# Performance work log

Hardware: AMD Instinct MI355X
Metric: run time of the kernel (lower is better)

The kernel has to match this reference:

```python
import jax, jax.numpy as jnp
import numpy as np

# R-FCN PSRoI pooling constants (match init_kwargs)
P = 7          # pooled_height == pooled_width
GS = 7         # group_size
D = 21         # output_dim
SCALE = 0.0625 # spatial_scale (1/16)


def setup_inputs() -> dict:
    key = jax.random.key(0)
    k1, k2, k3, k4 = jax.random.split(key, 4)
    N, C, H, W = 4, D * GS * GS, 80, 80   # C = output_dim * group_size^2
    R = 2048
    features = jax.random.normal(k1, (N, C, H, W), dtype=jnp.float32)
    img = H / SCALE  # 1280 px image
    bidx = jax.random.randint(k2, (R,), 0, N).astype(jnp.float32)
    xy1 = jax.random.uniform(k3, (R, 2), minval=0.0, maxval=img * 0.6)
    wh = jax.random.uniform(k4, (R, 2), minval=img * 0.05, maxval=img * 0.4)
    xy2 = jnp.clip(xy1 + wh, 0.0, img - 1.0)
    rois = jnp.concatenate([bidx[:, None], xy1, xy2], axis=1)  # [R,5]: (b,x1,y1,x2,y2)
    return {"features": features, "rois": rois}


def reference(features, rois):
    """Position-sensitive RoI pooling (R-FCN psroi_pooling_forward_cuda semantics).

    Each output bin (ctop, ph, pw) averages feature channel
    c = (ctop*GS + gh)*GS + gw over the bin's integer pixel region.
    Bin sums are computed exactly via a 2D integral image, turning the
    irregular per-bin reduction into 4 gathers per bin.
    """
    N, C, H, W = features.shape
    R = rois.shape[0]

    # Integral image: ii[n,c,i,j] = sum of features[n,c,:i,:j]; shape [N,C,H+1,W+1]
    ii = jnp.pad(
        jnp.cumsum(jnp.cumsum(features, axis=2), axis=3),
        ((0, 0), (0, 0), (1, 0), (1, 0)),
    )

    b = rois[:, 0].astype(jnp.int32)                       # [R]
    x1 = jnp.round(rois[:, 1]) * SCALE
    y1 = jnp.round(rois[:, 2]) * SCALE
    x2 = (jnp.round(rois[:, 3]) + 1.0) * SCALE
    y2 = (jnp.round(rois[:, 4]) + 1.0) * SCALE
    bin_w = jnp.maximum(x2 - x1, 0.1) / P                  # [R]
    bin_h = jnp.maximum(y2 - y1, 0.1) / P

    g = jnp.arange(P, dtype=jnp.float32)                   # bin index grid
    hs = jnp.clip(jnp.floor(g[None, :] * bin_h[:, None] + y1[:, None]), 0, H).astype(jnp.int32)        # [R,P]
    he = jnp.clip(jnp.ceil((g[None, :] + 1.0) * bin_h[:, None] + y1[:, None]), 0, H).astype(jnp.int32)
    ws = jnp.clip(jnp.floor(g[None, :] * bin_w[:, None] + x1[:, None]), 0, W).astype(jnp.int32)
    we = jnp.clip(jnp.ceil((g[None, :] + 1.0) * bin_w[:, None] + x1[:, None]), 0, W).astype(jnp.int32)

    # Position-sensitive channel map: c[ctop,ph,pw] = (ctop*GS+gh)*GS+gw
    ctop = jnp.arange(D)[:, None, None]
    gh = jnp.clip((jnp.arange(P) * GS) // P, 0, GS - 1)[None, :, None]
    gw = jnp.clip((jnp.arange(P) * GS) // P, 0, GS - 1)[None, None, :]
    cmap = (ctop * GS + gh) * GS + gw                      # [D,P,P]

    # Broadcast gather indices to [R,D,P,P]
    B = b[:, None, None, None]
    Cc = cmap[None]
    HS = hs[:, None, :, None]; HE = he[:, None, :, None]
    WS = ws[:, None, None, :]; WE = we[:, None, None, :]

    s = ii[B, Cc, HE, WE] - ii[B, Cc, HS, WE] - ii[B, Cc, HE, WS] + ii[B, Cc, HS, WS]
    area = ((HE - HS) * (WE - WS)).astype(features.dtype)
    out = jnp.where(area > 0, s / jnp.maximum(area, 1.0), jnp.zeros((), features.dtype))
    return out  # [R, D, P, P]
```

## Files before the change

### kernel.cpp

```cpp
#include <hip/hip_runtime.h>

#define P   7
#define GS  7
#define D   21
#define HH  80
#define WW  80
#define CC  (D * GS * GS)
#define PLANE (HH * WW)
#define IW  84
#define NSEG 5
#define SEGLEN 16

__device__ __forceinline__ float recip7() {
    union { unsigned u; float f; } c; c.u = 0x3E124925u; return c.f;
}

__device__ __forceinline__ float mul_add_nofma(float a, float b, float c) {
    float t = a * b;
    asm volatile("" : "+v"(t));
    return t + c;
}

__global__ __launch_bounds__(1024) void prep_kernel(
    const float* __restrict__ rois, int R, int N,
    unsigned short* __restrict__ hshe,
    unsigned short* __restrict__ wswe,
    int* __restrict__ jlist, int* __restrict__ base)
{
    __shared__ unsigned char bsh[2048];
    __shared__ int wcnt[16][8];
    __shared__ int wbase[16][8];
    __shared__ int baseS[9];
    int tid = threadIdx.x, wave = tid >> 6, lane = tid & 63;

    for (int r = tid; r < R; r += 1024) {
        const float* roi = rois + (size_t)r * 5;
        bsh[r] = (unsigned char)(int)roi[0];

        float x1 = rintf(roi[1]) * 0.0625f;
        float y1 = rintf(roi[2]) * 0.0625f;
        float x2 = (rintf(roi[3]) + 1.0f) * 0.0625f;
        float y2 = (rintf(roi[4]) + 1.0f) * 0.0625f;
        float bin_w = fmaxf(x2 - x1, 0.1f) * recip7();
        float bin_h = fmaxf(y2 - y1, 0.1f) * recip7();
        asm volatile("" : "+v"(bin_w), "+v"(bin_h));

        #pragma unroll
        for (int g = 0; g < 7; ++g) {
            float hs_f = floorf(mul_add_nofma((float)g,       bin_h, y1));
            float he_f = ceilf (mul_add_nofma((float)(g + 1), bin_h, y1));
            float ws_f = floorf(mul_add_nofma((float)g,       bin_w, x1));
            float we_f = ceilf (mul_add_nofma((float)(g + 1), bin_w, x1));
            int hs = (int)fminf(fmaxf(hs_f, 0.0f), 80.0f);
            int he = (int)fminf(fmaxf(he_f, 0.0f), 80.0f);
            int ws = (int)fminf(fmaxf(ws_f, 0.0f), 80.0f);
            int we = (int)fminf(fmaxf(we_f, 0.0f), 80.0f);
            hshe[r * 7 + g] = (unsigned short)(hs | (he << 8));
            wswe[r * 7 + g] = (unsigned short)(ws | (we << 8));
        }
    }
    __syncthreads();

    int chunk = (R + 15) / 16;
    int rbeg = wave * chunk;
    int rend = min(rbeg + chunk, R);
    int cnt[8];
    #pragma unroll
    for (int b = 0; b < 8; ++b) cnt[b] = 0;
    for (int rr = rbeg + lane; rr < rend; rr += 64) {
        int bv = bsh[rr];
        #pragma unroll
        for (int b = 0; b < 8; ++b) {
            if (b < N) cnt[b] += __popcll(__ballot(bv == b));
        }
    }
    if (lane == 0) {
        #pragma unroll
        for (int b = 0; b < 8; ++b) wcnt[wave][b] = cnt[b];
    }
    __syncthreads();

    if (tid < 8) {
        int b = tid, acc = 0;
        for (int w = 0; w < 16; ++w) { wbase[w][b] = acc; acc += wcnt[w][b]; }
        baseS[b] = acc;
    }
    __syncthreads();
    if (tid == 0) {
        int acc = 0;
        for (int b = 0; b < N; ++b) { int t = baseS[b]; baseS[b] = acc; acc += t; }
        baseS[N] = acc;
    }
    __syncthreads();

    {
        int off[8];
        #pragma unroll
        for (int b = 0; b < 8; ++b) off[b] = (b < N) ? (baseS[b] + wbase[wave][b]) : 0;
        for (int rr = rbeg + lane; rr < rend; rr += 64) {
            int bv = bsh[rr];
            #pragma unroll
            for (int b = 0; b < 8; ++b) {
                if (b < N) {
                    unsigned long long mask = __ballot(bv == b);
                    if (bv == b) {
                        int pos = off[b] + __popcll(mask & ((1ull << lane) - 1ull));
                        jlist[pos] = rr;
                    }
                    off[b] += __popcll(mask);
                }
            }
        }
    }
    if (tid <= N) base[tid] = baseS[tid];
}

__global__ __launch_bounds__(512) void psroi_plane_kernel(
    const float* __restrict__ feat, int R,
    const unsigned short* __restrict__ hshe,
    const unsigned short* __restrict__ wswe,
    const int* __restrict__ jlist, const int* __restrict__ base,
    float* __restrict__ dst)
{
    __shared__ float ii[HH * IW];
    __shared__ float tot[NSEG][HH];

    int tid = threadIdx.x;
    int bid = blockIdx.x;
    int b   = bid / CC;
    int c   = bid % CC;
    int rem = c % (GS * GS);
    int gh  = rem / GS;
    int gw  = rem % GS;

    const float4* src4 = (const float4*)(feat + ((size_t)b * CC + c) * PLANE);
    for (int i = tid; i < PLANE / 4; i += 512) {
        float4 v = src4[i];
        int h = i / 20;
        int w = (i % 20) * 4;
        *(float4*)(&ii[h * IW + w]) = v;
    }

    int j0 = base[b], j1 = base[b + 1];
    int jA = j0 + tid, jB = jA + 512, jC = jA + 1024, jD = jA + 1536;
    int rA = (jA < j1) ? jlist[jA] : 0;
    int rB = (jB < j1) ? jlist[jB] : 0;
    int rC = (jC < j1) ? jlist[jC] : 0;
    int rD = (jD < j1) ? jlist[jD] : 0;
    unsigned hA = (jA < j1) ? hshe[rA * 7 + gh] : 0;
    unsigned wA = (jA < j1) ? wswe[rA * 7 + gw] : 0;
    unsigned hB = (jB < j1) ? hshe[rB * 7 + gh] : 0;
    unsigned wB = (jB < j1) ? wswe[rB * 7 + gw] : 0;
    unsigned hC = (jC < j1) ? hshe[rC * 7 + gh] : 0;
    unsigned wC = (jC < j1) ? wswe[rC * 7 + gw] : 0;
    unsigned hD = (jD < j1) ? hshe[rD * 7 + gh] : 0;
    unsigned wD = (jD < j1) ? wswe[rD * 7 + gw] : 0;

    __syncthreads();

    bool act = tid < NSEG * WW;
    int seg = tid / WW;
    int lw  = tid % WW;

    {
        float v[SEGLEN];
        int col = lw, h0 = seg * SEGLEN;
        if (act) {
            float s = 0.0f;
            #pragma unroll
            for (int k = 0; k < SEGLEN; ++k) { v[k] = ii[(h0 + k) * IW + col]; s += v[k]; }
            tot[seg][lw] = s;
        }
        __syncthreads();
        if (act) {
            float off = 0.0f;
            #pragma unroll
            for (int jj = 0; jj < NSEG - 1; ++jj) if (jj < seg) off += tot[jj][lw];
            float run = off;
            #pragma unroll
            for (int k = 0; k < SEGLEN; ++k) { run += v[k]; ii[(h0 + k) * IW + col] = run; }
        }
        __syncthreads();
    }
    {
        float4 q0, q1, q2, q3;
        int row = lw, w0 = seg * SEGLEN;
        float4* rp = (float4*)&ii[row * IW + w0];
        if (act) {
            q0 = rp[0]; q1 = rp[1]; q2 = rp[2]; q3 = rp[3];
            float s = (((((q0.x + q0.y) + (q0.z + q0.w))
                       + ((q1.x + q1.y) + (q1.z + q1.w)))
                      + (((q2.x + q2.y) + (q2.z + q2.w))
                       + ((q3.x + q3.y) + (q3.z + q3.w)))));
            s = q0.x; s += q0.y; s += q0.z; s += q0.w;
            s += q1.x; s += q1.y; s += q1.z; s += q1.w;
            s += q2.x; s += q2.y; s += q2.z; s += q2.w;
            s += q3.x; s += q3.y; s += q3.z; s += q3.w;
            tot[seg][row] = s;
        }
        __syncthreads();
        if (act) {
            float off = 0.0f;
            #pragma unroll
            for (int jj = 0; jj < NSEG - 1; ++jj) if (jj < seg) off += tot[jj][row];
            float run = off;
            run += q0.x; q0.x = run; run += q0.y; q0.y = run;
            run += q0.z; q0.z = run; run += q0.w; q0.w = run;
            run += q1.x; q1.x = run; run += q1.y; q1.y = run;
            run += q1.z; q1.z = run; run += q1.w; q1.w = run;
            run += q2.x; q2.x = run; run += q2.y; q2.y = run;
            run += q2.z; q2.z = run; run += q2.w; q2.w = run;
            run += q3.x; q3.x = run; run += q3.y; q3.y = run;
            run += q3.z; q3.z = run; run += q3.w; q3.w = run;
            rp[0] = q0; rp[1] = q1; rp[2] = q2; rp[3] = q3;
        }
        __syncthreads();
    }

    #define IIV(hq, wq) ( ((hq) > 0 && (wq) > 0)                              \
        ? ii[((hq) - 1) * IW + ((wq) - 1)] : 0.0f )
    #define EMIT(jX, hX, wX)                                                  \
    if (jX < j1) {                                                            \
        int hs = hX & 255, he = (int)(hX >> 8);                               \
        int ws = wX & 255, we = (int)(wX >> 8);                               \
        float s = ((IIV(he, we) - IIV(hs, we))                                \
                 -  IIV(he, ws)) + IIV(hs, ws);                               \
        int area = (he - hs) * (we - ws);                                     \
        dst[(size_t)c * R + jX] = (area > 0) ? (s / (float)area) : 0.0f;      \
    }
    EMIT(jA, hA, wA)
    EMIT(jB, hB, wB)
    EMIT(jC, hC, wC)
    EMIT(jD, hD, wD)
    #undef EMIT
    #undef IIV
}

__global__ __launch_bounds__(256) void transpose_kernel(
    const float* __restrict__ in, const int* __restrict__ jlist,
    float* __restrict__ out, int R, int C)
{
    __shared__ float t[64][65];
    __shared__ int rows[64];
    int j0 = blockIdx.x * 64;
    int c0 = blockIdx.y * 64;
    int tx = threadIdx.x, ty = threadIdx.y;
    int tid = ty * 64 + tx;

    if (tid < 64 && j0 + tid < R) rows[tid] = jlist[j0 + tid];

    #pragma unroll
    for (int k0 = 0; k0 < 64; k0 += 4) {
        int k = k0 + ty;
        int cc = c0 + k, jj = j0 + tx;
        if (cc < C && jj < R) t[k][tx] = in[(size_t)cc * R + jj];
    }
    __syncthreads();
    #pragma unroll
    for (int k0 = 0; k0 < 64; k0 += 4) {
        int k = k0 + ty;
        int cc = c0 + tx;
        if (j0 + k < R && cc < C) out[(size_t)rows[k] * C + cc] = t[tx][k];
    }
}

__global__ __launch_bounds__(256) void psroi_fallback_kernel(
    const float* __restrict__ feat, const float* __restrict__ rois,
    int R, float* __restrict__ out)
{
    __shared__ float ii[81 * 81];
    int bid = blockIdx.x;
    int b = bid / CC, c = bid % CC;
    int rem = c % 49, gh = rem / 7, gw = rem % 7;

    const float* plane = feat + ((size_t)b * CC + c) * PLANE;
    for (int i = threadIdx.x; i < PLANE; i += 256) {
        int h = i / WW, w = i % WW;
        ii[(h + 1) * 81 + (w + 1)] = plane[i];
    }
    for (int i = threadIdx.x; i < 81; i += 256) { ii[i] = 0.0f; ii[i * 81] = 0.0f; }
    __syncthreads();
    if (threadIdx.x < WW) {
        int w = threadIdx.x + 1; float s = 0.0f;
        for (int h = 1; h <= HH; ++h) { s += ii[h * 81 + w]; ii[h * 81 + w] = s; }
    }
    __syncthreads();
    if (threadIdx.x < HH) {
        int h = threadIdx.x + 1; float* row = &ii[h * 81]; float s = 0.0f;
        for (int w = 1; w <= WW; ++w) { s += row[w]; row[w] = s; }
    }
    __syncthreads();
    for (int r = threadIdx.x; r < R; r += 256) {
        const float* roi = rois + (size_t)r * 5;
        if ((int)roi[0] != b) continue;
        float x1 = rintf(roi[1]) * 0.0625f;
        float y1 = rintf(roi[2]) * 0.0625f;
        float x2 = (rintf(roi[3]) + 1.0f) * 0.0625f;
        float y2 = (rintf(roi[4]) + 1.0f) * 0.0625f;
        float bw = fmaxf(x2 - x1, 0.1f) * recip7();
        float bh = fmaxf(y2 - y1, 0.1f) * recip7();
        asm volatile("" : "+v"(bw), "+v"(bh));
        int hs = (int)fminf(fmaxf(floorf(mul_add_nofma((float)gh,     bh, y1)), 0.0f), 80.0f);
        int he = (int)fminf(fmaxf(ceilf (mul_add_nofma((float)(gh+1), bh, y1)), 0.0f), 80.0f);
        int ws = (int)fminf(fmaxf(floorf(mul_add_nofma((float)gw,     bw, x1)), 0.0f), 80.0f);
        int we = (int)fminf(fmaxf(ceilf (mul_add_nofma((float)(gw+1), bw, x1)), 0.0f), 80.0f);
        float s = ii[he * 81 + we] - ii[hs * 81 + we] - ii[he * 81 + ws] + ii[hs * 81 + ws];
        int area = (he - hs) * (we - ws);
        out[(size_t)r * CC + c] = (area > 0) ? (s / (float)area) : 0.0f;
    }
}

extern "C" void kernel_launch(void* const* d_in, const int* in_sizes, int n_in,
                              void* d_out, int out_size, void* d_ws, size_t ws_size,
                              hipStream_t stream)
{
    const float* feat = (const float*)d_in[0];
    const float* rois = (const float*)d_in[1];
    float* out        = (float*)d_out;

    int R = in_sizes[1] / 5;
    int N = in_sizes[0] / (CC * PLANE);

    size_t off_wsT  = 0;
    size_t off_hshe = (off_wsT + (size_t)CC * R * sizeof(float) + 15) & ~(size_t)15;
    size_t off_wswe = off_hshe + (size_t)R * 7 * sizeof(unsigned short);
    size_t off_jl   = (off_wswe + (size_t)R * 7 * sizeof(unsigned short) + 15) & ~(size_t)15;
    size_t off_base = off_jl + (size_t)R * sizeof(int);
    size_t need     = off_base + (size_t)(N + 1) * sizeof(int);

    bool chunk_ok = (((R + 15) / 16) % 64) == 0;

    if (ws_size >= need && N <= 8 && R <= 2048 && chunk_ok) {
        char* ws = (char*)d_ws;
        float*          ws_T = (float*)(ws + off_wsT);
        unsigned short* hshe = (unsigned short*)(ws + off_hshe);
        unsigned short* wswe = (unsigned short*)(ws + off_wswe);
        int*            jl   = (int*)(ws + off_jl);
        int*            base = (int*)(ws + off_base);

        prep_kernel<<<1, 1024, 0, stream>>>(rois, R, N, hshe, wswe, jl, base);
        psroi_plane_kernel<<<N * CC, 512, 0, stream>>>(feat, R, hshe, wswe, jl, base, ws_T);
        dim3 blk(64, 4), grd((R + 63) / 64, (CC + 63) / 64);
        transpose_kernel<<<grd, blk, 0, stream>>>(ws_T, jl, out, R, CC);
    } else {
        psroi_fallback_kernel<<<N * CC, 256, 0, stream>>>(feat, rois, R, out);
    }
}
```

Baseline: 45.58 us.

## Make plane kernel persistent with double-buffered async global-to-LDS loads

Replaces the one-block-per-plane launch with 512 persistent blocks that each loop over several feature planes. The next plane is prefetched into a second LDS buffer with global_load_lds while the current plane is scanned and its bins are gathered. Barriers are replaced by manual s_waitcnt plus s_barrier. The aim is to hide global load latency behind the scan and gather work. In exchange LDS use per block roughly doubles, which lowers occupancy, and correctness now depends on hand-placed vmcnt waits.

```diff
diff --git a/kernel.cpp b/kernel.cpp
--- a/kernel.cpp
+++ b/kernel.cpp
@@ -10,6 +10,10 @@
 #define IW  84
 #define NSEG 5
 #define SEGLEN 16
+#define NBLK 512
+#define BUFQ 2048
+#define BUFF (BUFQ * 4)
+#define REALQ 1680
 
 __device__ __forceinline__ float recip7() {
     union { unsigned u; float f; } c; c.u = 0x3E124925u; return c.f;
@@ -19,6 +23,28 @@
     float t = a * b;
     asm volatile("" : "+v"(t));
     return t + c;
+}
+
+#define MEMFENCE() asm volatile("" ::: "memory")
+#define LGKM_BAR() do { asm volatile("s_waitcnt lgkmcnt(0)" ::: "memory"); \
+                        __builtin_amdgcn_s_barrier(); MEMFENCE(); } while (0)
+
+__device__ __forceinline__ void gll16(const float* g, float* l) {
+    __builtin_amdgcn_global_load_lds(
+        (const __attribute__((address_space(1))) void*)g,
+        (__attribute__((address_space(3))) void*)l, 16, 0, 0);
+}
+
+__device__ __forceinline__ void stage_issue(const float* plane, float* buf, int tid) {
+    #pragma unroll
+    for (int k = 0; k < 4; ++k) {
+        int q0 = (tid & ~63) + k * 512;
+        int q  = q0 + (tid & 63);
+        int row = q / 21, w4 = q - row * 21;
+        const float* src = (q < REALQ && w4 < 20) ? (plane + row * WW + w4 * 4)
+                                                  : plane;
+        gll16(src, buf + q0 * 4);
+    }
 }
 
 __global__ __launch_bounds__(1024) void prep_kernel(
@@ -116,124 +142,129 @@
 }
 
 __global__ __launch_bounds__(512) void psroi_plane_kernel(
-    const float* __restrict__ feat, int R,
+    const float* __restrict__ feat, int R, int NPLANES,
     const unsigned short* __restrict__ hshe,
     const unsigned short* __restrict__ wswe,
     const int* __restrict__ jlist, const int* __restrict__ base,
     float* __restrict__ dst)
 {
-    __shared__ float ii[HH * IW];
+    __shared__ float bufA[BUFF];
+    __shared__ float bufB[BUFF];
     __shared__ float tot[NSEG][HH];
 
     int tid = threadIdx.x;
     int bid = blockIdx.x;
-    int b   = bid / CC;
-    int c   = bid % CC;
-    int rem = c % (GS * GS);
-    int gh  = rem / GS;
-    int gw  = rem % GS;
-
-    const float4* src4 = (const float4*)(feat + ((size_t)b * CC + c) * PLANE);
-    for (int i = tid; i < PLANE / 4; i += 512) {
-        float4 v = src4[i];
-        int h = i / 20;
-        int w = (i % 20) * 4;
-        *(float4*)(&ii[h * IW + w]) = v;
-    }
-
-    int j0 = base[b], j1 = base[b + 1];
-    int jA = j0 + tid, jB = jA + 512, jC = jA + 1024, jD = jA + 1536;
-    int rA = (jA < j1) ? jlist[jA] : 0;
-    int rB = (jB < j1) ? jlist[jB] : 0;
-    int rC = (jC < j1) ? jlist[jC] : 0;
-    int rD = (jD < j1) ? jlist[jD] : 0;
-    unsigned hA = (jA < j1) ? hshe[rA * 7 + gh] : 0;
-    unsigned wA = (jA < j1) ? wswe[rA * 7 + gw] : 0;
-    unsigned hB = (jB < j1) ? hshe[rB * 7 + gh] : 0;
-    unsigned wB = (jB < j1) ? wswe[rB * 7 + gw] : 0;
-    unsigned hC = (jC < j1) ? hshe[rC * 7 + gh] : 0;
-    unsigned wC = (jC < j1) ? wswe[rC * 7 + gw] : 0;
-    unsigned hD = (jD < j1) ? hshe[rD * 7 + gh] : 0;
-    unsigned wD = (jD < j1) ? wswe[rD * 7 + gw] : 0;
-
-    __syncthreads();
+
+    stage_issue(feat + (size_t)bid * PLANE, bufA, tid);
 
     bool act = tid < NSEG * WW;
     int seg = tid / WW;
     int lw  = tid % WW;
 
-    {
-        float v[SEGLEN];
-        int col = lw, h0 = seg * SEGLEN;
-        if (act) {
-            float s = 0.0f;
-            #pragma unroll
-            for (int k = 0; k < SEGLEN; ++k) { v[k] = ii[(h0 + k) * IW + col]; s += v[k]; }
-            tot[seg][lw] = s;
-        }
-        __syncthreads();
-        if (act) {
-            float off = 0.0f;
-            #pragma unroll
-            for (int jj = 0; jj < NSEG - 1; ++jj) if (jj < seg) off += tot[jj][lw];
-            float run = off;
-            #pragma unroll
-            for (int k = 0; k < SEGLEN; ++k) { run += v[k]; ii[(h0 + k) * IW + col] = run; }
-        }
-        __syncthreads();
-    }
-    {
-        float4 q0, q1, q2, q3;
-        int row = lw, w0 = seg * SEGLEN;
-        float4* rp = (float4*)&ii[row * IW + w0];
-        if (act) {
-            q0 = rp[0]; q1 = rp[1]; q2 = rp[2]; q3 = rp[3];
-            float s = (((((q0.x + q0.y) + (q0.z + q0.w))
-                       + ((q1.x + q1.y) + (q1.z + q1.w)))
-                      + (((q2.x + q2.y) + (q2.z + q2.w))
-                       + ((q3.x + q3.y) + (q3.z + q3.w)))));
-            s = q0.x; s += q0.y; s += q0.z; s += q0.w;
-            s += q1.x; s += q1.y; s += q1.z; s += q1.w;
-            s += q2.x; s += q2.y; s += q2.z; s += q2.w;
-            s += q3.x; s += q3.y; s += q3.z; s += q3.w;
-            tot[seg][row] = s;
-        }
-        __syncthreads();
-        if (act) {
-            float off = 0.0f;
-            #pragma unroll
-            for (int jj = 0; jj < NSEG - 1; ++jj) if (jj < seg) off += tot[jj][row];
-            float run = off;
-            run += q0.x; q0.x = run; run += q0.y; q0.y = run;
-            run += q0.z; q0.z = run; run += q0.w; q0.w = run;
-            run += q1.x; q1.x = run; run += q1.y; q1.y = run;
-            run += q1.z; q1.z = run; run += q1.w; q1.w = run;
-            run += q2.x; q2.x = run; run += q2.y; q2.y = run;
-            run += q2.z; q2.z = run; run += q2.w; q2.w = run;
-            run += q3.x; q3.x = run; run += q3.y; q3.y = run;
-            run += q3.z; q3.z = run; run += q3.w; q3.w = run;
-            rp[0] = q0; rp[1] = q1; rp[2] = q2; rp[3] = q3;
-        }
-        __syncthreads();
-    }
-
-    #define IIV(hq, wq) ( ((hq) > 0 && (wq) > 0)                              \
-        ? ii[((hq) - 1) * IW + ((wq) - 1)] : 0.0f )
-    #define EMIT(jX, hX, wX)                                                  \
-    if (jX < j1) {                                                            \
-        int hs = hX & 255, he = (int)(hX >> 8);                               \
-        int ws = wX & 255, we = (int)(wX >> 8);                               \
-        float s = ((IIV(he, we) - IIV(hs, we))                                \
-                 -  IIV(he, ws)) + IIV(hs, ws);                               \
-        int area = (he - hs) * (we - ws);                                     \
-        dst[(size_t)c * R + jX] = (area > 0) ? (s / (float)area) : 0.0f;      \
-    }
-    EMIT(jA, hA, wA)
-    EMIT(jB, hB, wB)
-    EMIT(jC, hC, wC)
-    EMIT(jD, hD, wD)
-    #undef EMIT
-    #undef IIV
+    int parity = 0;
+    for (int p = bid; p < NPLANES; p += NBLK, parity ^= 1) {
+        float* ii = parity ? bufB : bufA;
+        float* nx = parity ? bufA : bufB;
+        int pn = p + NBLK;
+        if (pn < NPLANES) {
+            stage_issue(feat + (size_t)pn * PLANE, nx, tid);
+            asm volatile("s_waitcnt vmcnt(4)" ::: "memory");
+        } else {
+            asm volatile("s_waitcnt vmcnt(0)" ::: "memory");
+        }
+        __builtin_amdgcn_s_barrier();
+        MEMFENCE();
+
+        int b = p / CC, c = p % CC;
+        int rem = c % (GS * GS);
+        int gh  = rem / GS, gw = rem % GS;
+        int j0 = base[b], j1 = base[b + 1];
+        int jA = j0 + tid, jB = jA + 512, jC = jA + 1024, jD = jA + 1536;
+        int rA = (jA < j1) ? jlist[jA] : 0;
+        int rB = (jB < j1) ? jlist[jB] : 0;
+        int rC = (jC < j1) ? jlist[jC] : 0;
+        int rD = (jD < j1) ? jlist[jD] : 0;
+        unsigned hA = (jA < j1) ? hshe[rA * 7 + gh] : 0;
+        unsigned wA = (jA < j1) ? wswe[rA * 7 + gw] : 0;
+        unsigned hB = (jB < j1) ? hshe[rB * 7 + gh] : 0;
+        unsigned wB = (jB < j1) ? wswe[rB * 7 + gw] : 0;
+        unsigned hC = (jC < j1) ? hshe[rC * 7 + gh] : 0;
+        unsigned wC = (jC < j1) ? wswe[rC * 7 + gw] : 0;
+        unsigned hD = (jD < j1) ? hshe[rD * 7 + gh] : 0;
+        unsigned wD = (jD < j1) ? wswe[rD * 7 + gw] : 0;
+
+        {
+            float v[SEGLEN];
+            int col = lw, h0 = seg * SEGLEN;
+            if (act) {
+                float s = 0.0f;
+                #pragma unroll
+                for (int k = 0; k < SEGLEN; ++k) { v[k] = ii[(h0 + k) * IW + col]; s += v[k]; }
+                tot[seg][lw] = s;
+            }
+            LGKM_BAR();
+            if (act) {
+                float off = 0.0f;
+                #pragma unroll
+                for (int jj = 0; jj < NSEG - 1; ++jj) if (jj < seg) off += tot[jj][lw];
+                float run = off;
+                #pragma unroll
+                for (int k = 0; k < SEGLEN; ++k) { run += v[k]; ii[(h0 + k) * IW + col] = run; }
+            }
+            LGKM_BAR();
+        }
+        {
+            float4 q0, q1, q2, q3;
+            int row = lw, w0 = seg * SEGLEN;
+            float4* rp = (float4*)&ii[row * IW + w0];
+            if (act) {
+                q0 = rp[0]; q1 = rp[1]; q2 = rp[2]; q3 = rp[3];
+                float s;
+                s  = q0.x; s += q0.y; s += q0.z; s += q0.w;
+                s += q1.x; s += q1.y; s += q1.z; s += q1.w;
+                s += q2.x; s += q2.y; s += q2.z; s += q2.w;
+                s += q3.x; s += q3.y; s += q3.z; s += q3.w;
+                tot[seg][row] = s;
+            }
+            LGKM_BAR();
+            if (act) {
+                float off = 0.0f;
+                #pragma unroll
+                for (int jj = 0; jj < NSEG - 1; ++jj) if (jj < seg) off += tot[jj][row];
+                float run = off;
+                run += q0.x; q0.x = run; run += q0.y; q0.y = run;
+                run += q0.z; q0.z = run; run += q0.w; q0.w = run;
+                run += q1.x; q1.x = run; run += q1.y; q1.y = run;
+                run += q1.z; q1.z = run; run += q1.w; q1.w = run;
+                run += q2.x; q2.x = run; run += q2.y; q2.y = run;
+                run += q2.z; q2.z = run; run += q2.w; q2.w = run;
+                run += q3.x; q3.x = run; run += q3.y; q3.y = run;
+                run += q3.z; q3.z = run; run += q3.w; q3.w = run;
+                rp[0] = q0; rp[1] = q1; rp[2] = q2; rp[3] = q3;
+            }
+            LGKM_BAR();
+        }
+
+        #define IIV(hq, wq) ( ((hq) > 0 && (wq) > 0)                              \
+            ? ii[((hq) - 1) * IW + ((wq) - 1)] : 0.0f )
+        #define EMIT(jX, hX, wX)                                                  \
+        if (jX < j1) {                                                            \
+            int hs = hX & 255, he = (int)(hX >> 8);                               \
+            int ws = wX & 255, we = (int)(wX >> 8);                               \
+            float s = ((IIV(he, we) - IIV(hs, we))                                \
+                     -  IIV(he, ws)) + IIV(hs, ws);                               \
+            int area = (he - hs) * (we - ws);                                     \
+            dst[(size_t)c * R + jX] = (area > 0) ? (s / (float)area) : 0.0f;      \
+        }
+        EMIT(jA, hA, wA)
+        EMIT(jB, hB, wB)
+        EMIT(jC, hC, wC)
+        EMIT(jD, hD, wD)
+        #undef EMIT
+        #undef IIV
+
+        LGKM_BAR();
+    }
 }
 
 __global__ __launch_bounds__(256) void transpose_kernel(
@@ -320,6 +351,7 @@
 
     int R = in_sizes[1] / 5;
     int N = in_sizes[0] / (CC * PLANE);
+    int NPLANES = N * CC;
 
     size_t off_wsT  = 0;
     size_t off_hshe = (off_wsT + (size_t)CC * R * sizeof(float) + 15) & ~(size_t)15;
@@ -330,7 +362,7 @@
 
     bool chunk_ok = (((R + 15) / 16) % 64) == 0;
 
-    if (ws_size >= need && N <= 8 && R <= 2048 && chunk_ok) {
+    if (ws_size >= need && N <= 8 && R <= 2048 && chunk_ok && NPLANES > NBLK) {
         char* ws = (char*)d_ws;
         float*          ws_T = (float*)(ws + off_wsT);
         unsigned short* hshe = (unsigned short*)(ws + off_hshe);
@@ -339,10 +371,11 @@
         int*            base = (int*)(ws + off_base);
 
         prep_kernel<<<1, 1024, 0, stream>>>(rois, R, N, hshe, wswe, jl, base);
-        psroi_plane_kernel<<<N * CC, 512, 0, stream>>>(feat, R, hshe, wswe, jl, base, ws_T);
+        psroi_plane_kernel<<<NBLK, 512, 0, stream>>>(
+            feat, R, NPLANES, hshe, wswe, jl, base, ws_T);
         dim3 blk(64, 4), grd((R + 63) / 64, (CC + 63) / 64);
         transpose_kernel<<<grd, blk, 0, stream>>>(ws_T, jl, out, R, CC);
     } else {
-        psroi_fallback_kernel<<<N * CC, 256, 0, stream>>>(feat, rois, R, out);
-    }
-}
+        psroi_fallback_kernel<<<NPLANES, 256, 0, stream>>>(feat, rois, R, out);
+    }
+}
```

Result: slower. 51.78 us (+13.6%).

## Sort RoIs by batch and y-coordinate bucket via counting sort

Applied to the files above, without the earlier changes.

Replaces the per-batch stable compaction in the prep kernel with a counting sort keyed on (batch, y1/16 bucket), built from a shared-memory histogram, a block-wide scan and atomic scatter. The RoI order inside each batch is no longer stable, but RoIs with similar y positions end up adjacent. This probably aims for better locality or more uniform work per wave in the plane kernel. It also drops the chunk_ok launch restriction and removes a dead float sum in the plane kernel.

```diff
diff --git a/kernel.cpp b/kernel.cpp
--- a/kernel.cpp
+++ b/kernel.cpp
@@ -28,14 +28,23 @@
     int* __restrict__ jlist, int* __restrict__ base)
 {
     __shared__ unsigned char bsh[2048];
-    __shared__ int wcnt[16][8];
-    __shared__ int wbase[16][8];
-    __shared__ int baseS[9];
-    int tid = threadIdx.x, wave = tid >> 6, lane = tid & 63;
+    __shared__ unsigned char keyS[2048];
+    __shared__ int cntS[1024];
+    __shared__ int scanS[1024];
+    __shared__ int cursS[1024];
+    int tid = threadIdx.x;
+
+    cntS[tid] = 0;
+    __syncthreads();
 
     for (int r = tid; r < R; r += 1024) {
         const float* roi = rois + (size_t)r * 5;
-        bsh[r] = (unsigned char)(int)roi[0];
+        int b = (int)roi[0];
+        bsh[r] = (unsigned char)b;
+        int k = ((int)rintf(roi[2])) >> 4;
+        k = (k < 0) ? 0 : ((k > 127) ? 127 : k);
+        keyS[r] = (unsigned char)k;
+        atomicAdd(&cntS[b * 128 + k], 1);
 
         float x1 = rintf(roi[1]) * 0.0625f;
         float y1 = rintf(roi[2]) * 0.0625f;
@@ -61,58 +70,25 @@
     }
     __syncthreads();
 
-    int chunk = (R + 15) / 16;
-    int rbeg = wave * chunk;
-    int rend = min(rbeg + chunk, R);
-    int cnt[8];
-    #pragma unroll
-    for (int b = 0; b < 8; ++b) cnt[b] = 0;
-    for (int rr = rbeg + lane; rr < rend; rr += 64) {
-        int bv = bsh[rr];
-        #pragma unroll
-        for (int b = 0; b < 8; ++b) {
-            if (b < N) cnt[b] += __popcll(__ballot(bv == b));
-        }
-    }
-    if (lane == 0) {
-        #pragma unroll
-        for (int b = 0; b < 8; ++b) wcnt[wave][b] = cnt[b];
-    }
-    __syncthreads();
-
-    if (tid < 8) {
-        int b = tid, acc = 0;
-        for (int w = 0; w < 16; ++w) { wbase[w][b] = acc; acc += wcnt[w][b]; }
-        baseS[b] = acc;
-    }
-    __syncthreads();
-    if (tid == 0) {
-        int acc = 0;
-        for (int b = 0; b < N; ++b) { int t = baseS[b]; baseS[b] = acc; acc += t; }
-        baseS[N] = acc;
-    }
-    __syncthreads();
-
-    {
-        int off[8];
-        #pragma unroll
-        for (int b = 0; b < 8; ++b) off[b] = (b < N) ? (baseS[b] + wbase[wave][b]) : 0;
-        for (int rr = rbeg + lane; rr < rend; rr += 64) {
-            int bv = bsh[rr];
-            #pragma unroll
-            for (int b = 0; b < 8; ++b) {
-                if (b < N) {
-                    unsigned long long mask = __ballot(bv == b);
-                    if (bv == b) {
-                        int pos = off[b] + __popcll(mask & ((1ull << lane) - 1ull));
-                        jlist[pos] = rr;
-                    }
-                    off[b] += __popcll(mask);
-                }
-            }
-        }
-    }
-    if (tid <= N) base[tid] = baseS[tid];
+    scanS[tid] = cntS[tid];
+    __syncthreads();
+    for (int d = 1; d < 1024; d <<= 1) {
+        int add = (tid >= d) ? scanS[tid - d] : 0;
+        __syncthreads();
+        scanS[tid] += add;
+        __syncthreads();
+    }
+    int excl = scanS[tid] - cntS[tid];
+    cursS[tid] = excl;
+    __syncthreads();
+
+    if (tid < N) base[tid] = cursS[tid * 128];
+    if (tid == N) base[N] = scanS[1023];
+
+    for (int r = tid; r < R; r += 1024) {
+        int pos = atomicAdd(&cursS[bsh[r] * 128 + keyS[r]], 1);
+        jlist[pos] = r;
+    }
 }
 
 __global__ __launch_bounds__(512) void psroi_plane_kernel(
@@ -188,11 +164,8 @@
         float4* rp = (float4*)&ii[row * IW + w0];
         if (act) {
             q0 = rp[0]; q1 = rp[1]; q2 = rp[2]; q3 = rp[3];
-            float s = (((((q0.x + q0.y) + (q0.z + q0.w))
-                       + ((q1.x + q1.y) + (q1.z + q1.w)))
-                      + (((q2.x + q2.y) + (q2.z + q2.w))
-                       + ((q3.x + q3.y) + (q3.z + q3.w)))));
-            s = q0.x; s += q0.y; s += q0.z; s += q0.w;
+            float s;
+            s  = q0.x; s += q0.y; s += q0.z; s += q0.w;
             s += q1.x; s += q1.y; s += q1.z; s += q1.w;
             s += q2.x; s += q2.y; s += q2.z; s += q2.w;
             s += q3.x; s += q3.y; s += q3.z; s += q3.w;
@@ -328,9 +301,7 @@
     size_t off_base = off_jl + (size_t)R * sizeof(int);
     size_t need     = off_base + (size_t)(N + 1) * sizeof(int);
 
-    bool chunk_ok = (((R + 15) / 16) % 64) == 0;
-
-    if (ws_size >= need && N <= 8 && R <= 2048 && chunk_ok) {
+    if (ws_size >= need && N <= 8 && R <= 2048) {
         char* ws = (char*)d_ws;
         float*          ws_T = (float*)(ws + off_wsT);
         unsigned short* hshe = (unsigned short*)(ws + off_hshe);
```

Measured after the change: 47.86 us. 1.05x slower.
